# Kernel tuning notes

Hardware: AMD Instinct MI355X
Metric: run time of the kernel (lower is better)

Reference implementation:

```python
import jax, jax.numpy as jnp
import numpy as np

B, S, D, H = 2, 4096, 1024, 16
HD = D // H  # 64
BASE = 10000.0


def setup_inputs() -> dict:
    key = jax.random.key(0)
    ks = jax.random.split(key, 11)
    s = 1.0 / np.sqrt(D)
    return {
        "consulta": jax.random.normal(ks[0], (B, S, D), jnp.float32),
        "chave": jax.random.normal(ks[1], (B, S, D), jnp.float32),
        "valor": jax.random.normal(ks[2], (B, S, D), jnp.float32),
        "Wq": jax.random.normal(ks[3], (D, D), jnp.float32) * s,
        "bq": jnp.zeros((D,), jnp.float32),
        "Wk": jax.random.normal(ks[4], (D, D), jnp.float32) * s,
        "bk": jnp.zeros((D,), jnp.float32),
        "Wv": jax.random.normal(ks[5], (D, D), jnp.float32) * s,
        "bv": jnp.zeros((D,), jnp.float32),
        "Wo": jax.random.normal(ks[6], (D, D), jnp.float32) * s,
        "bo": jnp.zeros((D,), jnp.float32),
    }


def _rope(x):
    # x: [B, H, S, HD]; rotate interleaved (even, odd) pairs
    seq = x.shape[2]
    theta = 1.0 / (BASE ** (jnp.arange(0, HD, 2, dtype=jnp.float32) / HD))  # [HD/2]
    angles = jnp.arange(seq, dtype=jnp.float32)[:, None] * theta[None, :]  # [S, HD/2]
    cos, sin = jnp.cos(angles), jnp.sin(angles)
    xr = x.reshape(*x.shape[:-1], HD // 2, 2)
    x_re, x_im = xr[..., 0], xr[..., 1]
    out_re = x_re * cos - x_im * sin
    out_im = x_re * sin + x_im * cos
    return jnp.stack([out_re, out_im], axis=-1).reshape(x.shape)


def reference(consulta, chave, valor, Wq, bq, Wk, bk, Wv, bv, Wo, bo):
    b, s, _ = consulta.shape
    # projections (torch Linear: x @ W.T + b)
    Q = consulta @ Wq.T + bq
    K = chave @ Wk.T + bk
    V = valor @ Wv.T + bv
    # [B, H, S, HD]
    Q = Q.reshape(b, s, H, HD).transpose(0, 2, 1, 3)
    K = K.reshape(b, s, H, HD).transpose(0, 2, 1, 3)
    V = V.reshape(b, s, H, HD).transpose(0, 2, 1, 3)
    Q = _rope(Q)
    K = _rope(K)
    scores = jnp.einsum('bhqd,bhkd->bhqk', Q, K) / jnp.sqrt(jnp.float32(HD))
    weights = jax.nn.softmax(scores, axis=-1)  # dropout p=0 -> identity
    out = jnp.einsum('bhqk,bhkd->bhqd', weights, V)
    out = out.transpose(0, 2, 1, 3).reshape(b, s, D)
    return out @ Wo.T + bo
```

## Files before the change

### kernel.cpp

```cpp
#include <hip/hip_runtime.h>
#include <hip/hip_bf16.h>

typedef __attribute__((ext_vector_type(8))) short short8;
typedef __attribute__((ext_vector_type(4))) float f32x4;
typedef __attribute__((ext_vector_type(16))) float f32x16;
typedef __attribute__((ext_vector_type(4))) unsigned short ushort4v;
typedef __attribute__((ext_vector_type(4))) float float4v;
typedef __attribute__((ext_vector_type(2))) unsigned int uint32x2;
typedef __attribute__((ext_vector_type(4))) unsigned int uint32x4;

#define NB 2
#define NS 4096
#define ND 1024
#define NH 16
#define NHD 64

#define QSCALE 0.18033688011112042f

__device__ __forceinline__ unsigned short f2bf(float x) {
    union { float f; unsigned u; } v; v.f = x;
    unsigned r = v.u + 0x7FFFu + ((v.u >> 16) & 1u);
    return (unsigned short)(r >> 16);
}

__device__ __forceinline__ unsigned cvt_pk_bf16(float lo, float hi) {
    unsigned r;
    asm("v_cvt_pk_bf16_f32 %0, %1, %2" : "=v"(r) : "v"(lo), "v"(hi));
    return r;
}

__device__ __forceinline__ void gload_lds16(const unsigned short* g, unsigned short* l) {
    __builtin_amdgcn_global_load_lds(
        (const __attribute__((address_space(1))) void*)g,
        (__attribute__((address_space(3))) void*)l,
        16, 0, 0);
}

__global__ void rope_table_kernel(float* __restrict__ cosT, float* __restrict__ sinT) {
    int i = blockIdx.x * blockDim.x + threadIdx.x;
    int p = i & 31, s = i >> 5;
    float theta = exp2f(-(float)(2 * p) * (13.287712379549449f / 64.0f));
    float ang = (float)s * theta;
    float sv, cv;
    sincosf(ang, &sv, &cv);
    cosT[i] = cv; sinT[i] = sv;
}

__global__ void cast_bf16_kernel(const float* __restrict__ in, unsigned short* __restrict__ out, int n8) {
    int i = blockIdx.x * blockDim.x + threadIdx.x;
    if (i >= n8) return;
    float4v a0 = *(const float4v*)(&in[(size_t)i * 8]);
    float4v a1 = *(const float4v*)(&in[(size_t)i * 8 + 4]);
    short8 s8;
    s8[0] = (short)f2bf(a0.x); s8[1] = (short)f2bf(a0.y);
    s8[2] = (short)f2bf(a0.z); s8[3] = (short)f2bf(a0.w);
    s8[4] = (short)f2bf(a1.x); s8[5] = (short)f2bf(a1.y);
    s8[6] = (short)f2bf(a1.z); s8[7] = (short)f2bf(a1.w);
    *(short8*)(&out[(size_t)i * 8]) = s8;
}

template<int EPI>
__global__ __launch_bounds__(256, 2) void gemm_kernel(
    const unsigned short* __restrict__ A,
    const unsigned short* __restrict__ Wb,
    const float* __restrict__ bias,
    void* __restrict__ outv,
    const float* __restrict__ cosT,
    const float* __restrict__ sinT,
    float oscale)
{
    __shared__ unsigned short As[128 * 32];
    __shared__ unsigned short Bs[128 * 32];
    const int t = threadIdx.x;
    const int wave = t >> 6, lane = t & 63;
    const int quad = lane >> 4, l15 = lane & 15;
    const int wm = (wave & 1) * 64, wn = (wave >> 1) * 64;
    const int m0 = blockIdx.y * 128, n0 = blockIdx.x * 128;

    f32x4 acc[4][4];
#pragma unroll
    for (int i = 0; i < 4; i++)
#pragma unroll
        for (int j = 0; j < 4; j++)
            acc[i][j] = f32x4{0.f, 0.f, 0.f, 0.f};

    for (int k0 = 0; k0 < ND; k0 += 32) {
#pragma unroll
        for (int p = 0; p < 2; p++) {
            int idx = p * 256 + t;
            int r = idx >> 2, c = (idx & 3) * 8;
            unsigned short* ldsA = &As[(size_t)(p * 256 + wave * 64) * 8];
            unsigned short* ldsB = &Bs[(size_t)(p * 256 + wave * 64) * 8];
            gload_lds16(&A[(size_t)(m0 + r) * ND + k0 + c], ldsA);
            gload_lds16(&Wb[(size_t)(n0 + r) * ND + k0 + c], ldsB);
        }
        __syncthreads();

        short8 af[4], bfr[4];
#pragma unroll
        for (int mt = 0; mt < 4; mt++)
            af[mt] = *(const short8*)(&As[(wm + mt * 16 + l15) * 32 + quad * 8]);
#pragma unroll
        for (int nt = 0; nt < 4; nt++)
            bfr[nt] = *(const short8*)(&Bs[(wn + nt * 16 + l15) * 32 + quad * 8]);
#pragma unroll
        for (int mt = 0; mt < 4; mt++)
#pragma unroll
            for (int nt = 0; nt < 4; nt++) {
                if (EPI == 0)
                    acc[mt][nt] = __builtin_amdgcn_mfma_f32_16x16x32_bf16(bfr[nt], af[mt], acc[mt][nt], 0, 0, 0);
                else
                    acc[mt][nt] = __builtin_amdgcn_mfma_f32_16x16x32_bf16(af[mt], bfr[nt], acc[mt][nt], 0, 0, 0);
            }
        __syncthreads();
    }

    if (EPI == 0) {
        float* out = (float*)outv;
#pragma unroll
        for (int mt = 0; mt < 4; mt++) {
            int gm = m0 + wm + mt * 16 + l15;
#pragma unroll
            for (int nt = 0; nt < 4; nt++) {
                int gn0 = n0 + wn + nt * 16 + quad * 4;
                float4v fv;
#pragma unroll
                for (int r = 0; r < 4; r++)
                    fv[r] = acc[mt][nt][r] + bias[gn0 + r];
                *(float4v*)(&out[(size_t)gm * ND + gn0]) = fv;
            }
        }
    } else if (EPI == 1) {
        unsigned short* out = (unsigned short*)outv;
#pragma unroll
        for (int nt = 0; nt < 4; nt++) {
            int gn = n0 + wn + nt * 16 + l15;
            int h = gn >> 6, hd = gn & 63, pr = hd >> 1, im = gn & 1;
            float bv = bias[gn];
#pragma unroll
            for (int mt = 0; mt < 4; mt++) {
                int gm0 = m0 + wm + mt * 16 + quad * 4;
#pragma unroll
                for (int r = 0; r < 4; r++) {
                    int gm = gm0 + r;
                    int b = gm >> 12, s = gm & 4095;
                    float v = acc[mt][nt][r] + bv;
                    float pv = __shfl_xor(v, 1, 64);
                    float cv = cosT[s * 32 + pr], sv = sinT[s * 32 + pr];
                    float o = im ? (pv * sv + v * cv) : (v * cv - pv * sv);
                    out[((size_t)(b * NH + h) * NS + s) * NHD + hd] = f2bf(o * oscale);
                }
            }
        }
    } else {
        unsigned short* out = (unsigned short*)outv;
#pragma unroll
        for (int nt = 0; nt < 4; nt++) {
            int gn = n0 + wn + nt * 16 + l15;
            int h = gn >> 6, hd = gn & 63;
            float bv = bias[gn];
#pragma unroll
            for (int mt = 0; mt < 4; mt++) {
                int gm0 = m0 + wm + mt * 16 + quad * 4;
                int b = gm0 >> 12, s0 = gm0 & 4095;
                ushort4v pk;
#pragma unroll
                for (int r = 0; r < 4; r++)
                    pk[r] = f2bf(acc[mt][nt][r] + bv);
                *(ushort4v*)(&out[((size_t)(b * NH + h) * NHD + hd) * NS + s0]) = pk;
            }
        }
    }
}

__global__ __launch_bounds__(256, 2) void flash_kernel(
    const unsigned short* __restrict__ Qr,
    const unsigned short* __restrict__ Kr,
    const unsigned short* __restrict__ Vt,
    unsigned short* __restrict__ Yatt)
{
    __shared__ unsigned short Ks[128 * 72];
    __shared__ unsigned short Vs[64 * 136];
    const int t = threadIdx.x;
    const int wave = t >> 6, lane = t & 63;
    const int l31 = lane & 31, h = lane >> 5;
    const int bh = blockIdx.y;
    const int qb = blockIdx.x * 128;
    const int wq = wave * 32;
    const size_t base = (size_t)bh * NS * NHD;

    short8 qf[4];
#pragma unroll
    for (int ks = 0; ks < 4; ks++)
        qf[ks] = *(const short8*)(&Qr[base + (size_t)(qb + wq + l31) * NHD + ks * 16 + h * 8]);

    f32x16 accO[2];
#pragma unroll
    for (int dt = 0; dt < 2; dt++)
#pragma unroll
        for (int r = 0; r < 16; r++)
            accO[dt][r] = 0.f;
    float mrow = -1e30f, lrow = 0.f;

    for (int j0 = 0; j0 < NS; j0 += 128) {
#pragma unroll
        for (int p = 0; p < 4; p++) {
            int idx = p * 256 + t;
            { int r = idx >> 3, c = (idx & 7) * 8;
              *(short8*)(&Ks[r * 72 + c]) = *(const short8*)(&Kr[base + (size_t)(j0 + r) * NHD + c]); }
            { int r = idx >> 4, c = (idx & 15) * 8;
              *(short8*)(&Vs[r * 136 + c]) = *(const short8*)(&Vt[(size_t)(bh * NHD + r) * NS + j0 + c]); }
        }
        __syncthreads();

        f32x16 sa[4];
#pragma unroll
        for (int kt = 0; kt < 4; kt++)
#pragma unroll
            for (int r = 0; r < 16; r++)
                sa[kt][r] = 0.f;
        __builtin_amdgcn_s_setprio(1);
#pragma unroll
        for (int kt = 0; kt < 4; kt++)
#pragma unroll
            for (int ks = 0; ks < 4; ks++) {
                short8 ak = *(const short8*)(&Ks[(kt * 32 + l31) * 72 + ks * 16 + h * 8]);
                sa[kt] = __builtin_amdgcn_mfma_f32_32x32x16_bf16(ak, qf[ks], sa[kt], 0, 0, 0);
            }
        __builtin_amdgcn_s_setprio(0);

        float mx = -1e30f;
#pragma unroll
        for (int kt = 0; kt < 4; kt++) {
            float m0v = fmaxf(fmaxf(sa[kt][0], sa[kt][1]), fmaxf(sa[kt][2], sa[kt][3]));
            float m1v = fmaxf(fmaxf(sa[kt][4], sa[kt][5]), fmaxf(sa[kt][6], sa[kt][7]));
            float m2v = fmaxf(fmaxf(sa[kt][8], sa[kt][9]), fmaxf(sa[kt][10], sa[kt][11]));
            float m3v = fmaxf(fmaxf(sa[kt][12], sa[kt][13]), fmaxf(sa[kt][14], sa[kt][15]));
            mx = fmaxf(mx, fmaxf(fmaxf(m0v, m1v), fmaxf(m2v, m3v)));
        }
        mx = fmaxf(mx, __shfl_xor(mx, 32, 64));
        if (!__all(mx <= mrow + 8.0f)) {
            float mnew = fmaxf(mrow, mx);
            float alpha = exp2f(mrow - mnew);
            lrow *= alpha;
#pragma unroll
            for (int dt = 0; dt < 2; dt++)
#pragma unroll
                for (int r = 0; r < 16; r++)
                    accO[dt][r] *= alpha;
            mrow = mnew;
        }
        float ls0 = 0.f, ls1 = 0.f, ls2 = 0.f, ls3 = 0.f;
        unsigned pk[4][4][2];
#pragma unroll
        for (int kt = 0; kt < 4; kt++)
#pragma unroll
            for (int g = 0; g < 4; g++) {
                float p0 = exp2f(sa[kt][4 * g + 0] - mrow);
                float p1 = exp2f(sa[kt][4 * g + 1] - mrow);
                float p2 = exp2f(sa[kt][4 * g + 2] - mrow);
                float p3 = exp2f(sa[kt][4 * g + 3] - mrow);
                ls0 += p0; ls1 += p1; ls2 += p2; ls3 += p3;
                pk[kt][g][0] = cvt_pk_bf16(p0, p1);
                pk[kt][g][1] = cvt_pk_bf16(p2, p3);
            }
        float lsum = (ls0 + ls1) + (ls2 + ls3);
        lsum += __shfl_xor(lsum, 32, 64);
        lrow += lsum;

#pragma unroll
        for (int t2 = 0; t2 < 4; t2++)
#pragma unroll
            for (int u = 0; u < 2; u++)
#pragma unroll
                for (int j = 0; j < 2; j++)
                    asm volatile("v_permlane32_swap_b32 %0, %1"
                                 : "+v"(pk[t2][2 * u][j]), "+v"(pk[t2][2 * u + 1][j]));

        __builtin_amdgcn_s_setprio(1);
#pragma unroll
        for (int ks2 = 0; ks2 < 8; ks2++) {
            const int t2 = ks2 >> 1, u = ks2 & 1;
            uint32x4 bw;
            bw.x = pk[t2][2 * u][0];     bw.y = pk[t2][2 * u][1];
            bw.z = pk[t2][2 * u + 1][0]; bw.w = pk[t2][2 * u + 1][1];
            short8 bp = __builtin_bit_cast(short8, bw);
#pragma unroll
            for (int dt = 0; dt < 2; dt++) {
                short8 av = *(const short8*)(&Vs[(dt * 32 + l31) * 136 + ks2 * 16 + h * 8]);
                accO[dt] = __builtin_amdgcn_mfma_f32_32x32x16_bf16(av, bp, accO[dt], 0, 0, 0);
            }
        }
        __builtin_amdgcn_s_setprio(0);
        __syncthreads();
    }

    int b = bh >> 4, hh = bh & 15;
    float rl = 1.f / lrow;
    int s = qb + wq + l31;
#pragma unroll
    for (int dt = 0; dt < 2; dt++)
#pragma unroll
        for (int g = 0; g < 4; g++) {
            uint32x2 w;
            w.x = cvt_pk_bf16(accO[dt][4 * g + 0] * rl, accO[dt][4 * g + 1] * rl);
            w.y = cvt_pk_bf16(accO[dt][4 * g + 2] * rl, accO[dt][4 * g + 3] * rl);
            int d0 = dt * 32 + 8 * g + 4 * h;
            *(uint32x2*)(&Yatt[((size_t)(b * NS + s)) * ND + hh * NHD + d0]) = w;
        }
}

extern "C" void kernel_launch(void* const* d_in, const int* in_sizes, int n_in,
                              void* d_out, int out_size, void* d_ws, size_t ws_size,
                              hipStream_t stream) {
    const float* consulta = (const float*)d_in[0];
    const float* chave    = (const float*)d_in[1];
    const float* valor    = (const float*)d_in[2];
    const float* Wq = (const float*)d_in[3];
    const float* bq = (const float*)d_in[4];
    const float* Wk = (const float*)d_in[5];
    const float* bk = (const float*)d_in[6];
    const float* Wv = (const float*)d_in[7];
    const float* bv = (const float*)d_in[8];
    const float* Wo = (const float*)d_in[9];
    const float* bo = (const float*)d_in[10];

    const size_t NX = (size_t)8192 * 1024;

    float* cosT = (float*)d_ws;
    float* sinT = cosT + (size_t)NS * 32;
    unsigned short* Qrb = (unsigned short*)(sinT + (size_t)NS * 32);
    unsigned short* Krb = Qrb + NX;
    unsigned short* Vtb = Krb + NX;
    unsigned short* Yat = Vtb + NX;
    unsigned short* Abf = Yat + NX;
    unsigned short* Wbf = Abf + NX;

    rope_table_kernel<<<NS * 32 / 256, 256, 0, stream>>>(cosT, sinT);

    const int ACT8 = (int)(NX / 8);
    const int W8 = ND * ND / 8;

    dim3 ggrid(8, 64);

    cast_bf16_kernel<<<ACT8 / 256, 256, 0, stream>>>(consulta, Abf, ACT8);
    cast_bf16_kernel<<<W8 / 256, 256, 0, stream>>>(Wq, Wbf, W8);
    gemm_kernel<1><<<ggrid, 256, 0, stream>>>(Abf, Wbf, bq, Qrb, cosT, sinT, QSCALE);

    cast_bf16_kernel<<<ACT8 / 256, 256, 0, stream>>>(chave, Abf, ACT8);
    cast_bf16_kernel<<<W8 / 256, 256, 0, stream>>>(Wk, Wbf, W8);
    gemm_kernel<1><<<ggrid, 256, 0, stream>>>(Abf, Wbf, bk, Krb, cosT, sinT, 1.0f);

    cast_bf16_kernel<<<ACT8 / 256, 256, 0, stream>>>(valor, Abf, ACT8);
    cast_bf16_kernel<<<W8 / 256, 256, 0, stream>>>(Wv, Wbf, W8);
    gemm_kernel<2><<<ggrid, 256, 0, stream>>>(Abf, Wbf, bv, Vtb, cosT, sinT, 1.0f);

    flash_kernel<<<dim3(32, 32), 256, 0, stream>>>(Qrb, Krb, Vtb, Yat);

    cast_bf16_kernel<<<W8 / 256, 256, 0, stream>>>(Wo, Wbf, W8);
    gemm_kernel<0><<<ggrid, 256, 0, stream>>>(Yat, Wbf, bo, d_out, cosT, sinT, 1.0f);
}
```

Baseline: 518.4 us.

## Merge Q/K/V projections into one batched GEMM launch with staged bf16 inputs

Casts all three activations and weights into separate workspace buffers, then runs a single QKV GEMM with a 24x64 grid where the block's column range selects which projection and epilogue it handles. This is meant to fill the GPU better and remove the serial cast-then-GEMM dependency chain between the three projections. The code falls back to per-projection launches if the workspace is too small. It also raises the GEMM launch-bounds occupancy hint to 3 and has the flash score MFMA start from a zero accumulator instead of zero-filling it every tile. The cost is more workspace memory and runtime branching on which projection a block handles.

```diff
diff --git a/kernel.cpp b/kernel.cpp
--- a/kernel.cpp
+++ b/kernel.cpp
@@ -59,15 +59,116 @@
     *(short8*)(&out[(size_t)i * 8]) = s8;
 }
 
-template<int EPI>
-__global__ __launch_bounds__(256, 2) void gemm_kernel(
+__global__ __launch_bounds__(256, 3) void gemm_qkv_kernel(
+    const unsigned short* __restrict__ A0,
+    const unsigned short* __restrict__ A1,
+    const unsigned short* __restrict__ A2,
+    const unsigned short* __restrict__ W3,
+    const float* __restrict__ biasq,
+    const float* __restrict__ biask,
+    const float* __restrict__ biasv,
+    unsigned short* __restrict__ Qrb,
+    unsigned short* __restrict__ Krb,
+    unsigned short* __restrict__ Vtb,
+    const float* __restrict__ cosT,
+    const float* __restrict__ sinT,
+    int which_base)
+{
+    __shared__ unsigned short As[128 * 32];
+    __shared__ unsigned short Bs[128 * 32];
+    const int t = threadIdx.x;
+    const int wave = t >> 6, lane = t & 63;
+    const int quad = lane >> 4, l15 = lane & 15;
+    const int wm = (wave & 1) * 64, wn = (wave >> 1) * 64;
+    const int m0 = blockIdx.y * 128;
+    const int n0g = blockIdx.x * 128;
+    const int which = (n0g >> 10) + which_base;
+    const int n0 = n0g & 1023;
+    const unsigned short* A = (which == 0) ? A0 : (which == 1) ? A1 : A2;
+
+    f32x4 acc[4][4];
+#pragma unroll
+    for (int i = 0; i < 4; i++)
+#pragma unroll
+        for (int j = 0; j < 4; j++)
+            acc[i][j] = f32x4{0.f, 0.f, 0.f, 0.f};
+
+    for (int k0 = 0; k0 < ND; k0 += 32) {
+#pragma unroll
+        for (int p = 0; p < 2; p++) {
+            int idx = p * 256 + t;
+            int r = idx >> 2, c = (idx & 3) * 8;
+            unsigned short* ldsA = &As[(size_t)(p * 256 + wave * 64) * 8];
+            unsigned short* ldsB = &Bs[(size_t)(p * 256 + wave * 64) * 8];
+            gload_lds16(&A[(size_t)(m0 + r) * ND + k0 + c], ldsA);
+            gload_lds16(&W3[(size_t)(n0g + r) * ND + k0 + c], ldsB);
+        }
+        __syncthreads();
+
+        short8 af[4], bfr[4];
+#pragma unroll
+        for (int mt = 0; mt < 4; mt++)
+            af[mt] = *(const short8*)(&As[(wm + mt * 16 + l15) * 32 + quad * 8]);
+#pragma unroll
+        for (int nt = 0; nt < 4; nt++)
+            bfr[nt] = *(const short8*)(&Bs[(wn + nt * 16 + l15) * 32 + quad * 8]);
+#pragma unroll
+        for (int mt = 0; mt < 4; mt++)
+#pragma unroll
+            for (int nt = 0; nt < 4; nt++)
+                acc[mt][nt] = __builtin_amdgcn_mfma_f32_16x16x32_bf16(af[mt], bfr[nt], acc[mt][nt], 0, 0, 0);
+        __syncthreads();
+    }
+
+    if (which < 2) {
+        unsigned short* out = (which == 0) ? Qrb : Krb;
+        const float* bias = (which == 0) ? biasq : biask;
+        const float oscale = (which == 0) ? QSCALE : 1.0f;
+#pragma unroll
+        for (int nt = 0; nt < 4; nt++) {
+            int gn = n0 + wn + nt * 16 + l15;
+            int h = gn >> 6, hd = gn & 63, pr = hd >> 1, im = gn & 1;
+            float bvv = bias[gn];
+#pragma unroll
+            for (int mt = 0; mt < 4; mt++) {
+                int gm0 = m0 + wm + mt * 16 + quad * 4;
+#pragma unroll
+                for (int r = 0; r < 4; r++) {
+                    int gm = gm0 + r;
+                    int b = gm >> 12, s = gm & 4095;
+                    float v = acc[mt][nt][r] + bvv;
+                    float pv = __shfl_xor(v, 1, 64);
+                    float cv = cosT[s * 32 + pr], sv = sinT[s * 32 + pr];
+                    float o = im ? (pv * sv + v * cv) : (v * cv - pv * sv);
+                    out[((size_t)(b * NH + h) * NS + s) * NHD + hd] = f2bf(o * oscale);
+                }
+            }
+        }
+    } else {
+#pragma unroll
+        for (int nt = 0; nt < 4; nt++) {
+            int gn = n0 + wn + nt * 16 + l15;
+            int h = gn >> 6, hd = gn & 63;
+            float bvv = biasv[gn];
+#pragma unroll
+            for (int mt = 0; mt < 4; mt++) {
+                int gm0 = m0 + wm + mt * 16 + quad * 4;
+                int b = gm0 >> 12, s0 = gm0 & 4095;
+                ushort4v pk;
+#pragma unroll
+                for (int r = 0; r < 4; r++)
+                    pk[r] = f2bf(acc[mt][nt][r] + bvv);
+                *(ushort4v*)(&Vtb[((size_t)(b * NH + h) * NHD + hd) * NS + s0]) = pk;
+            }
+        }
+    }
+}
+
+__global__ __launch_bounds__(256, 2) void gemm_o_kernel(
     const unsigned short* __restrict__ A,
     const unsigned short* __restrict__ Wb,
     const float* __restrict__ bias,
-    void* __restrict__ outv,
-    const float* __restrict__ cosT,
-    const float* __restrict__ sinT,
-    float oscale)
+    float* __restrict__ out)
 {
     __shared__ unsigned short As[128 * 32];
     __shared__ unsigned short Bs[128 * 32];
@@ -106,69 +207,22 @@
 #pragma unroll
         for (int mt = 0; mt < 4; mt++)
 #pragma unroll
-            for (int nt = 0; nt < 4; nt++) {
-                if (EPI == 0)
-                    acc[mt][nt] = __builtin_amdgcn_mfma_f32_16x16x32_bf16(bfr[nt], af[mt], acc[mt][nt], 0, 0, 0);
-                else
-                    acc[mt][nt] = __builtin_amdgcn_mfma_f32_16x16x32_bf16(af[mt], bfr[nt], acc[mt][nt], 0, 0, 0);
-            }
-        __syncthreads();
-    }
-
-    if (EPI == 0) {
-        float* out = (float*)outv;
-#pragma unroll
-        for (int mt = 0; mt < 4; mt++) {
-            int gm = m0 + wm + mt * 16 + l15;
-#pragma unroll
-            for (int nt = 0; nt < 4; nt++) {
-                int gn0 = n0 + wn + nt * 16 + quad * 4;
-                float4v fv;
-#pragma unroll
-                for (int r = 0; r < 4; r++)
-                    fv[r] = acc[mt][nt][r] + bias[gn0 + r];
-                *(float4v*)(&out[(size_t)gm * ND + gn0]) = fv;
-            }
-        }
-    } else if (EPI == 1) {
-        unsigned short* out = (unsigned short*)outv;
+            for (int nt = 0; nt < 4; nt++)
+                acc[mt][nt] = __builtin_amdgcn_mfma_f32_16x16x32_bf16(bfr[nt], af[mt], acc[mt][nt], 0, 0, 0);
+        __syncthreads();
+    }
+
+#pragma unroll
+    for (int mt = 0; mt < 4; mt++) {
+        int gm = m0 + wm + mt * 16 + l15;
 #pragma unroll
         for (int nt = 0; nt < 4; nt++) {
-            int gn = n0 + wn + nt * 16 + l15;
-            int h = gn >> 6, hd = gn & 63, pr = hd >> 1, im = gn & 1;
-            float bv = bias[gn];
-#pragma unroll
-            for (int mt = 0; mt < 4; mt++) {
-                int gm0 = m0 + wm + mt * 16 + quad * 4;
-#pragma unroll
-                for (int r = 0; r < 4; r++) {
-                    int gm = gm0 + r;
-                    int b = gm >> 12, s = gm & 4095;
-                    float v = acc[mt][nt][r] + bv;
-                    float pv = __shfl_xor(v, 1, 64);
-                    float cv = cosT[s * 32 + pr], sv = sinT[s * 32 + pr];
-                    float o = im ? (pv * sv + v * cv) : (v * cv - pv * sv);
-                    out[((size_t)(b * NH + h) * NS + s) * NHD + hd] = f2bf(o * oscale);
-                }
-            }
-        }
-    } else {
-        unsigned short* out = (unsigned short*)outv;
-#pragma unroll
-        for (int nt = 0; nt < 4; nt++) {
-            int gn = n0 + wn + nt * 16 + l15;
-            int h = gn >> 6, hd = gn & 63;
-            float bv = bias[gn];
-#pragma unroll
-            for (int mt = 0; mt < 4; mt++) {
-                int gm0 = m0 + wm + mt * 16 + quad * 4;
-                int b = gm0 >> 12, s0 = gm0 & 4095;
-                ushort4v pk;
-#pragma unroll
-                for (int r = 0; r < 4; r++)
-                    pk[r] = f2bf(acc[mt][nt][r] + bv);
-                *(ushort4v*)(&out[((size_t)(b * NH + h) * NHD + hd) * NS + s0]) = pk;
-            }
+            int gn0 = n0 + wn + nt * 16 + quad * 4;
+            float4v fv;
+#pragma unroll
+            for (int r = 0; r < 4; r++)
+                fv[r] = acc[mt][nt][r] + bias[gn0 + r];
+            *(float4v*)(&out[(size_t)gm * ND + gn0]) = fv;
         }
     }
 }
@@ -194,12 +248,13 @@
     for (int ks = 0; ks < 4; ks++)
         qf[ks] = *(const short8*)(&Qr[base + (size_t)(qb + wq + l31) * NHD + ks * 16 + h * 8]);
 
+    f32x16 zacc;
+#pragma unroll
+    for (int r = 0; r < 16; r++)
+        zacc[r] = 0.f;
+
     f32x16 accO[2];
-#pragma unroll
-    for (int dt = 0; dt < 2; dt++)
-#pragma unroll
-        for (int r = 0; r < 16; r++)
-            accO[dt][r] = 0.f;
+    accO[0] = zacc; accO[1] = zacc;
     float mrow = -1e30f, lrow = 0.f;
 
     for (int j0 = 0; j0 < NS; j0 += 128) {
@@ -214,19 +269,18 @@
         __syncthreads();
 
         f32x16 sa[4];
-#pragma unroll
-        for (int kt = 0; kt < 4; kt++)
-#pragma unroll
-            for (int r = 0; r < 16; r++)
-                sa[kt][r] = 0.f;
         __builtin_amdgcn_s_setprio(1);
 #pragma unroll
-        for (int kt = 0; kt < 4; kt++)
-#pragma unroll
-            for (int ks = 0; ks < 4; ks++) {
+        for (int kt = 0; kt < 4; kt++) {
+            short8 ak0 = *(const short8*)(&Ks[(kt * 32 + l31) * 72 + h * 8]);
+            f32x16 s = __builtin_amdgcn_mfma_f32_32x32x16_bf16(ak0, qf[0], zacc, 0, 0, 0);
+#pragma unroll
+            for (int ks = 1; ks < 4; ks++) {
                 short8 ak = *(const short8*)(&Ks[(kt * 32 + l31) * 72 + ks * 16 + h * 8]);
-                sa[kt] = __builtin_amdgcn_mfma_f32_32x32x16_bf16(ak, qf[ks], sa[kt], 0, 0, 0);
+                s = __builtin_amdgcn_mfma_f32_32x32x16_bf16(ak, qf[ks], s, 0, 0, 0);
             }
+            sa[kt] = s;
+        }
         __builtin_amdgcn_s_setprio(0);
 
         float mx = -1e30f;
@@ -326,6 +380,10 @@
     const float* bo = (const float*)d_in[10];
 
     const size_t NX = (size_t)8192 * 1024;
+    const size_t NW = (size_t)ND * ND;
+
+    const int ACT8 = (int)(NX / 8);
+    const int W8 = (int)(NW / 8);
 
     float* cosT = (float*)d_ws;
     float* sinT = cosT + (size_t)NS * 32;
@@ -333,30 +391,48 @@
     unsigned short* Krb = Qrb + NX;
     unsigned short* Vtb = Krb + NX;
     unsigned short* Yat = Vtb + NX;
-    unsigned short* Abf = Yat + NX;
-    unsigned short* Wbf = Abf + NX;
+    unsigned short* A0  = Yat + NX;
+
+    const size_t need_merged =
+        (size_t)NS * 32 * 2 * sizeof(float) + (4 + 3) * NX * 2 + 3 * NW * 2;
+    const bool merged = ws_size >= need_merged;
 
     rope_table_kernel<<<NS * 32 / 256, 256, 0, stream>>>(cosT, sinT);
 
-    const int ACT8 = (int)(NX / 8);
-    const int W8 = ND * ND / 8;
-
-    dim3 ggrid(8, 64);
-
-    cast_bf16_kernel<<<ACT8 / 256, 256, 0, stream>>>(consulta, Abf, ACT8);
-    cast_bf16_kernel<<<W8 / 256, 256, 0, stream>>>(Wq, Wbf, W8);
-    gemm_kernel<1><<<ggrid, 256, 0, stream>>>(Abf, Wbf, bq, Qrb, cosT, sinT, QSCALE);
-
-    cast_bf16_kernel<<<ACT8 / 256, 256, 0, stream>>>(chave, Abf, ACT8);
-    cast_bf16_kernel<<<W8 / 256, 256, 0, stream>>>(Wk, Wbf, W8);
-    gemm_kernel<1><<<ggrid, 256, 0, stream>>>(Abf, Wbf, bk, Krb, cosT, sinT, 1.0f);
-
-    cast_bf16_kernel<<<ACT8 / 256, 256, 0, stream>>>(valor, Abf, ACT8);
-    cast_bf16_kernel<<<W8 / 256, 256, 0, stream>>>(Wv, Wbf, W8);
-    gemm_kernel<2><<<ggrid, 256, 0, stream>>>(Abf, Wbf, bv, Vtb, cosT, sinT, 1.0f);
-
-    flash_kernel<<<dim3(32, 32), 256, 0, stream>>>(Qrb, Krb, Vtb, Yat);
-
-    cast_bf16_kernel<<<W8 / 256, 256, 0, stream>>>(Wo, Wbf, W8);
-    gemm_kernel<0><<<ggrid, 256, 0, stream>>>(Yat, Wbf, bo, d_out, cosT, sinT, 1.0f);
-}
+    if (merged) {
+        unsigned short* A1 = A0 + NX;
+        unsigned short* A2 = A1 + NX;
+        unsigned short* W3 = A2 + NX;
+
+        cast_bf16_kernel<<<ACT8 / 256, 256, 0, stream>>>(consulta, A0, ACT8);
+        cast_bf16_kernel<<<ACT8 / 256, 256, 0, stream>>>(chave,    A1, ACT8);
+        cast_bf16_kernel<<<ACT8 / 256, 256, 0, stream>>>(valor,    A2, ACT8);
+        cast_bf16_kernel<<<W8 / 256, 256, 0, stream>>>(Wq, W3,          W8);
+        cast_bf16_kernel<<<W8 / 256, 256, 0, stream>>>(Wk, W3 + NW,     W8);
+        cast_bf16_kernel<<<W8 / 256, 256, 0, stream>>>(Wv, W3 + 2 * NW, W8);
+
+        gemm_qkv_kernel<<<dim3(24, 64), 256, 0, stream>>>(
+            A0, A1, A2, W3, bq, bk, bv, Qrb, Krb, Vtb, cosT, sinT, 0);
+
+        flash_kernel<<<dim3(32, 32), 256, 0, stream>>>(Qrb, Krb, Vtb, Yat);
+
+        cast_bf16_kernel<<<W8 / 256, 256, 0, stream>>>(Wo, W3, W8);
+        gemm_o_kernel<<<dim3(8, 64), 256, 0, stream>>>(Yat, W3, bo, (float*)d_out);
+    } else {
+        unsigned short* W3 = A0 + NX;
+
+        const float* acts[3]  = {consulta, chave, valor};
+        const float* ws[3]    = {Wq, Wk, Wv};
+        for (int i = 0; i < 3; i++) {
+            cast_bf16_kernel<<<ACT8 / 256, 256, 0, stream>>>(acts[i], A0, ACT8);
+            cast_bf16_kernel<<<W8 / 256, 256, 0, stream>>>(ws[i], W3, W8);
+            gemm_qkv_kernel<<<dim3(8, 64), 256, 0, stream>>>(
+                A0, A0, A0, W3, bq, bk, bv, Qrb, Krb, Vtb, cosT, sinT, i);
+        }
+
+        flash_kernel<<<dim3(32, 32), 256, 0, stream>>>(Qrb, Krb, Vtb, Yat);
+
+        cast_bf16_kernel<<<W8 / 256, 256, 0, stream>>>(Wo, W3, W8);
+        gemm_o_kernel<<<dim3(8, 64), 256, 0, stream>>>(Yat, W3, bo, (float*)d_out);
+    }
+}
```

Result: no change. 524.4 us (+1.2%).
